# Kernel optimization log

Hardware: AMD Instinct MI355X
Metric: run time of the kernel (lower is better)

The kernel has to match this reference:

```python
import jax, jax.numpy as jnp
import numpy as np

B, S, H = 32, 4096, 16
QC, LORA, ROPE, NOPE, VH, DM = 1536, 512, 64, 128, 128, 2048
SCALE = 1.0 / np.sqrt(NOPE + ROPE)


def _rope(x, pos):
    # GPT-NeoX style rotary, dim=ROPE, base=10000. x: [B,H,ROPE] or [B,ROPE]
    half = ROPE // 2
    inv = 1.0 / (10000.0 ** (jnp.arange(half, dtype=jnp.float32) / half))
    f = pos.astype(jnp.float32)[:, None] * inv  # [B, half]
    cos, sin = jnp.cos(f), jnp.sin(f)
    if x.ndim == 3:
        cos, sin = cos[:, None, :], sin[:, None, :]
    x1, x2 = x[..., :half], x[..., half:]
    return jnp.concatenate([x1 * cos - x2 * sin, x2 * cos + x1 * sin], axis=-1)


def setup_inputs() -> dict:
    key = jax.random.key(0)
    ks = jax.random.split(key, 11)
    w = 0.02  # small init so logits are well-scaled
    return {
        "q_c": jax.random.normal(ks[0], (B, QC), jnp.float32),
        "k_c_normed": jax.random.normal(ks[1], (B, LORA), jnp.float32),
        "k_pe": jax.random.normal(ks[2], (B, ROPE), jnp.float32),
        "kv_c_cache": jax.random.normal(ks[3], (B, S, LORA), jnp.float32),
        "k_pe_cache": jax.random.normal(ks[4], (B, S, ROPE), jnp.float32),
        "W_UQ": jax.random.normal(ks[5], (QC, H, NOPE), jnp.float32) * w,
        "W_UK": jax.random.normal(ks[6], (LORA, H, NOPE), jnp.float32) * w,
        "W_QR": jax.random.normal(ks[7], (QC, H * ROPE), jnp.float32) * w,
        "W_UV": jax.random.normal(ks[8], (LORA, H, VH), jnp.float32) * w,
        "W_O": jax.random.normal(ks[9], (H * VH, DM), jnp.float32) * w,
        "input_positions": jnp.full((B,), S - 1, dtype=jnp.int32),
    }


def reference(q_c, k_c_normed, k_pe, kv_c_cache, k_pe_cache,
              W_UQ, W_UK, W_QR, W_UV, W_O, input_positions):
    pos = input_positions
    # matrix-absorbed q_nope: (q_c @ W_UQ) absorbed through W_UK -> latent space
    q_t = jnp.einsum('bd,dhn->bhn', q_c, W_UQ)            # [B,H,NOPE]
    q_nope = jnp.einsum('bhn,lhn->bhl', q_t, W_UK)        # [B,H,LORA]
    q_pe = _rope((q_c @ W_QR).reshape(B, H, ROPE), pos)   # [B,H,ROPE]
    k_pe_rot = _rope(k_pe, pos)                            # [B,ROPE]
    # write current latent token into cache (paged write flattened)
    b_idx = jnp.arange(B)
    kv_c = kv_c_cache.at[b_idx, pos].set(k_c_normed)       # [B,S,LORA]
    kp = k_pe_cache.at[b_idx, pos].set(k_pe_rot)           # [B,S,ROPE]
    # attention in latent space
    scores = (jnp.einsum('bhl,bsl->bhs', q_nope, kv_c)
              + jnp.einsum('bhr,bsr->bhs', q_pe, kp)) * SCALE
    attn = jax.nn.softmax(scores, axis=-1)                 # [B,H,S]
    o = jnp.einsum('bhs,bsl->bhl', attn, kv_c)             # [B,H,LORA]
    v = jnp.einsum('bhl,lhv->bhv', o, W_UV)                # [B,H,VH]
    out = v.reshape(B, H * VH) @ W_O                       # [B,DM]
    return out.reshape(B, 1, DM)
```

## Files before the change

### kernel.cpp

```cpp
#include <hip/hip_runtime.h>
#include <hip/hip_bf16.h>
#include <math.h>

#define B 32
#define S 4096
#define H 16
#define QC 1536
#define LORA 512
#define ROPE 64
#define NOPE 128
#define VH 128
#define DM 2048
#define NC 32
#define CHUNK (S / NC)
#define NKS 24
#define FLP 584

__device__ __constant__ float SCALE_C = 0.07216878364870323f;

typedef __attribute__((ext_vector_type(8))) short bf16x8;
typedef __attribute__((ext_vector_type(4))) float f32x4;

__device__ inline ushort f2b(float x) {
    union { float f; uint u; } v; v.f = x;
    return (ushort)((v.u + 0x7FFFu + ((v.u >> 16) & 1u)) >> 16);
}

__global__ __launch_bounds__(256) void k_proj_part(
    const float* __restrict__ q_c, const float* __restrict__ W_UQ,
    const float* __restrict__ W_QR, float* __restrict__ part) {
    const int ks = blockIdx.x, cs = blockIdx.y, t = threadIdx.x;
    const int k0 = ks * 64;
    __shared__ float qs[64][32];
    for (int i = t; i < 64 * 32; i += 256) {
        const int k = i >> 5, b2 = i & 31;
        qs[k][b2] = q_c[(size_t)b2 * QC + k0 + k];
    }
    __syncthreads();
    const int tc = t & 63, tb = t >> 6;
    const int col = cs * 256 + tc * 4;
    const float* W; int N, coll;
    if (cs < 8) { W = W_UQ; N = 2048; coll = col; }
    else        { W = W_QR; N = 1024; coll = col - 2048; }
    float4 acc[8];
#pragma unroll
    for (int i = 0; i < 8; i++) acc[i] = make_float4(0.f, 0.f, 0.f, 0.f);
#pragma unroll 4
    for (int k = 0; k < 64; ++k) {
        const float4 w4 = *(const float4*)(W + (size_t)(k0 + k) * N + coll);
        const float4 a1 = *(const float4*)&qs[k][tb * 8];
        const float4 a2 = *(const float4*)&qs[k][tb * 8 + 4];
        acc[0].x += a1.x * w4.x; acc[0].y += a1.x * w4.y; acc[0].z += a1.x * w4.z; acc[0].w += a1.x * w4.w;
        acc[1].x += a1.y * w4.x; acc[1].y += a1.y * w4.y; acc[1].z += a1.y * w4.z; acc[1].w += a1.y * w4.w;
        acc[2].x += a1.z * w4.x; acc[2].y += a1.z * w4.y; acc[2].z += a1.z * w4.z; acc[2].w += a1.z * w4.w;
        acc[3].x += a1.w * w4.x; acc[3].y += a1.w * w4.y; acc[3].z += a1.w * w4.z; acc[3].w += a1.w * w4.w;
        acc[4].x += a2.x * w4.x; acc[4].y += a2.x * w4.y; acc[4].z += a2.x * w4.z; acc[4].w += a2.x * w4.w;
        acc[5].x += a2.y * w4.x; acc[5].y += a2.y * w4.y; acc[5].z += a2.y * w4.z; acc[5].w += a2.y * w4.w;
        acc[6].x += a2.z * w4.x; acc[6].y += a2.z * w4.y; acc[6].z += a2.z * w4.z; acc[6].w += a2.z * w4.w;
        acc[7].x += a2.w * w4.x; acc[7].y += a2.w * w4.y; acc[7].z += a2.w * w4.z; acc[7].w += a2.w * w4.w;
    }
#pragma unroll
    for (int j = 0; j < 8; j++) {
        const int b2 = tb * 8 + j;
        *(float4*)(part + ((size_t)ks * 32 + b2) * 3072 + col) = acc[j];
    }
}

__global__ __launch_bounds__(256) void k_finalize(
    const float* __restrict__ part, const float* __restrict__ k_pe,
    const int* __restrict__ pos_arr, float* __restrict__ q_t,
    ushort* __restrict__ q_bf, float* __restrict__ kpe_rot) {
    const int blk = blockIdx.x, t = threadIdx.x;
    if (blk < 64) {
        const int idx = blk * 256 + t;
        const int b = idx >> 9, c4 = idx & 511;
        const int col = c4 * 4;
        float4 acc = make_float4(0.f, 0.f, 0.f, 0.f);
        for (int ks = 0; ks < NKS; ks++) {
            const float4 p = *(const float4*)(part + ((size_t)ks * 32 + b) * 3072 + col);
            acc.x += p.x; acc.y += p.y; acc.z += p.z; acc.w += p.w;
        }
        *(float4*)(q_t + (size_t)b * 2048 + col) = acc;
    } else if (blk < 80) {
        const int idx = (blk - 64) * 256 + t;
        const int b = idx >> 7, rest = idx & 127;
        const int h = rest >> 3, pr = rest & 7;
        const int col1 = 2048 + h * 64 + pr * 4;
        float x1[4] = {0.f, 0.f, 0.f, 0.f}, x2[4] = {0.f, 0.f, 0.f, 0.f};
        for (int ks = 0; ks < NKS; ks++) {
            const float* p = part + ((size_t)ks * 32 + b) * 3072;
            const float4 a = *(const float4*)(p + col1);
            const float4 c = *(const float4*)(p + col1 + 32);
            x1[0] += a.x; x1[1] += a.y; x1[2] += a.z; x1[3] += a.w;
            x2[0] += c.x; x2[1] += c.y; x2[2] += c.z; x2[3] += c.w;
        }
        const int pos = pos_arr[b];
        ushort* qb = q_bf + ((size_t)b * 16 + h) * 576 + 512 + pr * 4;
#pragma unroll
        for (int e = 0; e < 4; ++e) {
            const int j = pr * 4 + e;
            const double inv = pow(10000.0, -(double)j / 32.0);
            const double f = (double)pos * inv;
            const float cc = (float)cos(f), ss = (float)sin(f);
            qb[e] = f2b(x1[e] * cc - x2[e] * ss);
            qb[32 + e] = f2b(x2[e] * cc + x1[e] * ss);
        }
    } else {
        for (int i = t; i < 32 * 32; i += 256) {
            const int b = i >> 5, j = i & 31;
            const int pos = pos_arr[b];
            const double inv = pow(10000.0, -(double)j / 32.0);
            const double f = (double)pos * inv;
            const float cc = (float)cos(f), ss = (float)sin(f);
            const float x1 = k_pe[(size_t)b * 64 + j], x2 = k_pe[(size_t)b * 64 + j + 32];
            kpe_rot[(size_t)b * 64 + j] = x1 * cc - x2 * ss;
            kpe_rot[(size_t)b * 64 + j + 32] = x2 * cc + x1 * ss;
        }
    }
}

__global__ __launch_bounds__(256) void k_qnope(
    const float* __restrict__ q_t, const float* __restrict__ W_UK,
    ushort* __restrict__ q_bf) {
    const int l0 = blockIdx.x * 64, h = blockIdx.y;
    const int t = threadIdx.x;
    __shared__ float qs[32][NOPE];
    for (int i = t; i < 32 * NOPE; i += 256) {
        const int b2 = i >> 7, n = i & 127;
        qs[b2][n] = q_t[(size_t)b2 * 2048 + h * NOPE + n];
    }
    __syncthreads();
    const int wave = t >> 6, lane = t & 63;
    const int half = lane >> 5, nl = (lane & 31) * 4;
    for (int sw = 0; sw < 8; ++sw) {
        const int l = l0 + sw * 8 + wave * 2 + half;
        const float4 w4 = *(const float4*)(W_UK + ((size_t)l * H + h) * NOPE + nl);
        for (int b2 = 0; b2 < 32; ++b2) {
            const float4 a4 = *(const float4*)&qs[b2][nl];
            float d = a4.x * w4.x + a4.y * w4.y + a4.z * w4.z + a4.w * w4.w;
            d += __shfl_xor(d, 16);
            d += __shfl_xor(d, 8);
            d += __shfl_xor(d, 4);
            d += __shfl_xor(d, 2);
            d += __shfl_xor(d, 1);
            if ((lane & 31) == 0)
                q_bf[((size_t)b2 * 16 + h) * 576 + l] = f2b(d);
        }
    }
}

__global__ __launch_bounds__(256) void k_flash(
    const ushort* __restrict__ q_bf, const float* __restrict__ kv_cache,
    const float* __restrict__ kpe_cache, const float* __restrict__ k_c_normed,
    const float* __restrict__ kpe_rot, const int* __restrict__ pos_arr,
    float* __restrict__ part_o, float* __restrict__ part_ml) {
    __shared__ ushort k_lds[2][16][FLP];
    __shared__ uint p_lds[4][16][20];
    const int blk = blockIdx.x;
    const int b = blk / NC, c = blk % NC;
    const int t = threadIdx.x, lane = t & 63, wave = t >> 6;
    const int lg = lane >> 4, hd = lane & 15;
    const int pos = pos_arr[b];
    const int s0 = c * CHUNK;
    const int rel = pos - s0;
    const int pt = (rel >= 0 && rel < CHUNK) ? (rel >> 4) : -1;
    const int prow = rel & 15;

    const float* kv_b = kv_cache + (size_t)b * S * LORA;
    const float* kp_b = kpe_cache + (size_t)b * S * ROPE;
    const float* kc_b = k_c_normed + (size_t)b * LORA;
    const float* kr_b = kpe_rot + (size_t)b * ROPE;

    bf16x8 qf[18];
    {
        const ushort* qr = q_bf + ((size_t)b * 16 + hd) * 576 + lg * 8;
#pragma unroll
        for (int ks = 0; ks < 18; ++ks)
            qf[ks] = *(const bf16x8*)(qr + 32 * ks);
    }

    float4 ld[9];
    auto issue = [&](int tile) {
        const int r = t >> 4, f0 = t & 15;
        const int s = s0 + tile * 16 + r;
        const float* kvr = kv_b + (size_t)s * LORA;
        const float* per = kp_b + (size_t)s * ROPE;
#pragma unroll
        for (int k = 0; k < 8; ++k) ld[k] = *(const float4*)(kvr + 4 * (f0 + 16 * k));
        ld[8] = *(const float4*)(per + 4 * f0);
    };
    auto wtile = [&](int buf) {
        const int r = t >> 4, f0 = t & 15;
        ushort* dst = &k_lds[buf][r][0];
#pragma unroll
        for (int k = 0; k < 9; ++k) {
            const int f = f0 + 16 * k;
            ushort4 h4;
            h4.x = f2b(ld[k].x); h4.y = f2b(ld[k].y);
            h4.z = f2b(ld[k].z); h4.w = f2b(ld[k].w);
            *(ushort4*)(dst + 4 * f) = h4;
        }
    };
    auto patch = [&](int buf) {
        if (t < 144) {
            const float4 v = (t < 128) ? *(const float4*)(kc_b + 4 * t)
                                       : *(const float4*)(kr_b + 4 * (t - 128));
            ushort4 h4;
            h4.x = f2b(v.x); h4.y = f2b(v.y); h4.z = f2b(v.z); h4.w = f2b(v.w);
            *(ushort4*)(&k_lds[buf][prow][4 * t]) = h4;
        }
    };

    f32x4 acc[8];
#pragma unroll
    for (int i = 0; i < 8; ++i) acc[i] = (f32x4){0.f, 0.f, 0.f, 0.f};
    float m_run = -INFINITY, l_run = 0.f;

    issue(0);
    wtile(0);
    if (pt == 0) patch(0);
    __syncthreads();

    for (int tt = 0; tt < 8; ++tt) {
        if (tt < 7) issue(tt + 1);

        f32x4 S4 = (f32x4){0.f, 0.f, 0.f, 0.f};
        {
            const ushort* krow = &k_lds[tt & 1][hd][lg * 8];
#pragma unroll
            for (int ks = 0; ks < 18; ++ks) {
                const bf16x8 av = *(const bf16x8*)(krow + 32 * ks);
                S4 = __builtin_amdgcn_mfma_f32_16x16x32_bf16(av, qf[ks], S4, 0, 0, 0);
            }
        }
        const float sc0 = S4[0] * SCALE_C, sc1 = S4[1] * SCALE_C;
        const float sc2 = S4[2] * SCALE_C, sc3 = S4[3] * SCALE_C;

        float smax = fmaxf(fmaxf(sc0, sc1), fmaxf(sc2, sc3));
        smax = fmaxf(smax, __shfl_xor(smax, 16));
        smax = fmaxf(smax, __shfl_xor(smax, 32));
        const bool need = smax > m_run + 8.0f;
        if (__any(need)) {
            const float m_new = need ? smax : m_run;
            const float alpha = __expf(m_run - m_new);
            l_run *= alpha;
            m_run = m_new;
            const int hb = lg * 4;
            const float a0 = __shfl(alpha, hb + 0), a1 = __shfl(alpha, hb + 1);
            const float a2 = __shfl(alpha, hb + 2), a3 = __shfl(alpha, hb + 3);
#pragma unroll
            for (int d2 = 0; d2 < 8; ++d2) {
                acc[d2][0] *= a0; acc[d2][1] *= a1;
                acc[d2][2] *= a2; acc[d2][3] *= a3;
            }
        }
        const float p0 = __expf(sc0 - m_run), p1 = __expf(sc1 - m_run);
        const float p2 = __expf(sc2 - m_run), p3 = __expf(sc3 - m_run);
        float ps = p0 + p1 + p2 + p3;
        ps += __shfl_xor(ps, 16);
        ps += __shfl_xor(ps, 32);
        l_run += ps;
        const uint plo = (uint)f2b(p0) | ((uint)f2b(p1) << 16);
        const uint phi = (uint)f2b(p2) | ((uint)f2b(p3) << 16);
        *(uint2*)&p_lds[wave][hd][(tt & 1) * 8 + lg * 2] = make_uint2(plo, phi);

        if (tt & 1) {
            const bf16x8 ap = *(const bf16x8*)&p_lds[wave][hd][lg * 4];
            const int half = lane >> 5;
            const int rbase = (lg & 1) * 8;
#pragma unroll
            for (int dt = 0; dt < 8; ++dt) {
                const int dcol = wave * 128 + dt * 16 + hd;
                union { bf16x8 v; ushort u[8]; } bv;
#pragma unroll
                for (int i2 = 0; i2 < 8; ++i2)
                    bv.u[i2] = k_lds[half][rbase + i2][dcol];
                acc[dt] = __builtin_amdgcn_mfma_f32_16x16x32_bf16(ap, bv.v, acc[dt], 0, 0, 0);
            }
        }

        __syncthreads();
        if (tt < 7) {
            wtile((tt + 1) & 1);
            if (pt == tt + 1) patch((tt + 1) & 1);
        }
        __syncthreads();
    }

    float* po = part_o + ((size_t)(b * NC + c) * H) * LORA;
#pragma unroll
    for (int dt = 0; dt < 8; ++dt) {
        const int dim = wave * 128 + dt * 16 + hd;
        const int hb = lg * 4;
        po[(size_t)(hb + 0) * LORA + dim] = acc[dt][0];
        po[(size_t)(hb + 1) * LORA + dim] = acc[dt][1];
        po[(size_t)(hb + 2) * LORA + dim] = acc[dt][2];
        po[(size_t)(hb + 3) * LORA + dim] = acc[dt][3];
    }
    if (wave == 0 && lane < 16) {
        float* pml = part_ml + ((size_t)(b * NC + c) * H + lane) * 2;
        pml[0] = m_run;
        pml[1] = l_run;
    }
}

__global__ __launch_bounds__(256) void k_combine(
    const float* __restrict__ part_o, const float* __restrict__ part_ml,
    const float* __restrict__ W_UV, float* __restrict__ v) {
    const int b0 = blockIdx.x * 4, h = blockIdx.y, t = threadIdx.x;
    __shared__ float ml_s[4][NC][2];
    __shared__ float o_s[4][LORA];
    if (t < 256) {
        const int b2 = t >> 6, c = (t >> 1) & 31, w = t & 1;
        ml_s[b2][c][w] = part_ml[(((size_t)(b0 + b2) * NC + c) * H + h) * 2 + w];
    }
    __syncthreads();
    float m_b[4], inv_l[4];
#pragma unroll
    for (int b2 = 0; b2 < 4; ++b2) {
        float m = -INFINITY;
        for (int c = 0; c < NC; c++) m = fmaxf(m, ml_s[b2][c][0]);
        float l = 0.f;
        for (int c = 0; c < NC; c++) l += ml_s[b2][c][1] * __expf(ml_s[b2][c][0] - m);
        m_b[b2] = m;
        inv_l[b2] = 1.0f / l;
    }
    for (int i = t; i < 4 * LORA; i += 256) {
        const int b2 = i >> 9, li = i & 511;
        float acc = 0.f;
        for (int c = 0; c < NC; c++) {
            acc += part_o[(((size_t)(b0 + b2) * NC + c) * H + h) * LORA + li] *
                   __expf(ml_s[b2][c][0] - m_b[b2]);
        }
        o_s[b2][li] = acc * inv_l[b2];
    }
    __syncthreads();
    const int vi = t & 127, bp = t >> 7;
    float acc0 = 0.f, acc1 = 0.f;
    for (int l = 0; l < LORA; l += 4) {
        const float w0 = W_UV[(size_t)(l + 0) * (H * VH) + h * VH + vi];
        const float w1 = W_UV[(size_t)(l + 1) * (H * VH) + h * VH + vi];
        const float w2 = W_UV[(size_t)(l + 2) * (H * VH) + h * VH + vi];
        const float w3 = W_UV[(size_t)(l + 3) * (H * VH) + h * VH + vi];
        const float4 oa = *(const float4*)&o_s[bp * 2][l];
        const float4 ob = *(const float4*)&o_s[bp * 2 + 1][l];
        acc0 += oa.x * w0 + oa.y * w1 + oa.z * w2 + oa.w * w3;
        acc1 += ob.x * w0 + ob.y * w1 + ob.z * w2 + ob.w * w3;
    }
    v[(size_t)(b0 + bp * 2) * (H * VH) + h * VH + vi] = acc0;
    v[(size_t)(b0 + bp * 2 + 1) * (H * VH) + h * VH + vi] = acc1;
}

__global__ void k_out(const float* __restrict__ v, const float* __restrict__ W_O,
                      float* __restrict__ out_part) {
    const int dsl = blockIdx.x, ksl = blockIdx.y, t = threadIdx.x;
    const int d0 = dsl * 128, k0 = ksl * 128;
    __shared__ float vs[32][128];
    for (int i = t; i < 32 * 128; i += 256) {
        const int bi = i >> 7, kk = i & 127;
        vs[bi][kk] = v[(size_t)bi * DM + k0 + kk];
    }
    __syncthreads();
    const int dl = t & 127, bh = t >> 7;
    float acc[16];
#pragma unroll
    for (int i = 0; i < 16; i++) acc[i] = 0.f;
    for (int kk = 0; kk < 128; kk += 4) {
        const float w0 = W_O[(size_t)(k0 + kk + 0) * DM + d0 + dl];
        const float w1 = W_O[(size_t)(k0 + kk + 1) * DM + d0 + dl];
        const float w2 = W_O[(size_t)(k0 + kk + 2) * DM + d0 + dl];
        const float w3 = W_O[(size_t)(k0 + kk + 3) * DM + d0 + dl];
#pragma unroll
        for (int i = 0; i < 16; i++) {
            const float4 vv = *(const float4*)&vs[bh * 16 + i][kk];
            acc[i] += vv.x * w0 + vv.y * w1 + vv.z * w2 + vv.w * w3;
        }
    }
    float* op = out_part + (size_t)ksl * 32 * DM;
#pragma unroll
    for (int i = 0; i < 16; i++) op[(size_t)(bh * 16 + i) * DM + d0 + dl] = acc[i];
}

__global__ void k_out_reduce(const float* __restrict__ out_part, float* __restrict__ out) {
    const int idx = blockIdx.x * 256 + threadIdx.x;
    float4 acc = make_float4(0.f, 0.f, 0.f, 0.f);
    for (int ks = 0; ks < 16; ks++) {
        float4 p = *(const float4*)(out_part + (size_t)ks * (32 * DM) + (size_t)idx * 4);
        acc.x += p.x; acc.y += p.y; acc.z += p.z; acc.w += p.w;
    }
    *(float4*)(out + (size_t)idx * 4) = acc;
}

extern "C" void kernel_launch(void* const* d_in, const int* in_sizes, int n_in,
                              void* d_out, int out_size, void* d_ws, size_t ws_size,
                              hipStream_t stream) {
    const float* q_c        = (const float*)d_in[0];
    const float* k_c_normed = (const float*)d_in[1];
    const float* k_pe       = (const float*)d_in[2];
    const float* kv_c_cache = (const float*)d_in[3];
    const float* k_pe_cache = (const float*)d_in[4];
    const float* W_UQ       = (const float*)d_in[5];
    const float* W_UK       = (const float*)d_in[6];
    const float* W_QR       = (const float*)d_in[7];
    const float* W_UV       = (const float*)d_in[8];
    const float* W_O        = (const float*)d_in[9];
    const int*   pos        = (const int*)d_in[10];

    float* ws = (float*)d_ws;
    float* q_t       = ws;
    float* qbf_f     = q_t + 65536;
    ushort* q_bf     = (ushort*)qbf_f;
    float* kpe_rot   = qbf_f + 147456;
    float* part_o    = kpe_rot + 2048;
    float* part_ml   = part_o + (size_t)B * NC * H * LORA;
    float* v         = part_ml + (size_t)B * NC * H * 2;
    float* out_part  = v + 65536;
    float* proj_part = out_part + (size_t)16 * 32 * DM;

    k_proj_part<<<dim3(NKS, 12), 256, 0, stream>>>(q_c, W_UQ, W_QR, proj_part);
    k_finalize<<<81, 256, 0, stream>>>(proj_part, k_pe, pos, q_t, q_bf, kpe_rot);
    k_qnope<<<dim3(8, 16), 256, 0, stream>>>(q_t, W_UK, q_bf);
    k_flash<<<B * NC, 256, 0, stream>>>(q_bf, kv_c_cache, k_pe_cache,
                                        k_c_normed, kpe_rot, pos, part_o, part_ml);
    k_combine<<<dim3(8, 16), 256, 0, stream>>>(part_o, part_ml, W_UV, v);
    k_out<<<dim3(16, 16), 256, 0, stream>>>(v, W_O, out_part);
    k_out_reduce<<<64, 256, 0, stream>>>(out_part, (float*)d_out);
}
```

Before: 226.4 us.

## Triple-buffer LDS tiles with two register prefetch sets in flash kernel

The flash-decode chunk loop now uses three LDS buffers and two register staging arrays, so the next tile is written to LDS right after the current tile's compute without an extra barrier. This removes one __syncthreads per tile and keeps global loads two tiles ahead. In exchange it uses more LDS and doubles the prefetch registers, which may lower occupancy.

```diff
diff --git a/kernel.cpp b/kernel.cpp
--- a/kernel.cpp
+++ b/kernel.cpp
@@ -154,7 +154,7 @@
     const float* __restrict__ kpe_cache, const float* __restrict__ k_c_normed,
     const float* __restrict__ kpe_rot, const int* __restrict__ pos_arr,
     float* __restrict__ part_o, float* __restrict__ part_ml) {
-    __shared__ ushort k_lds[2][16][FLP];
+    __shared__ ushort k_lds[3][16][FLP];
     __shared__ uint p_lds[4][16][20];
     const int blk = blockIdx.x;
     const int b = blk / NC, c = blk % NC;
@@ -179,8 +179,8 @@
             qf[ks] = *(const bf16x8*)(qr + 32 * ks);
     }
 
-    float4 ld[9];
-    auto issue = [&](int tile) {
+    float4 ldA[9], ldB[9];
+    auto issue = [&](int tile, float4 (&ld)[9]) {
         const int r = t >> 4, f0 = t & 15;
         const int s = s0 + tile * 16 + r;
         const float* kvr = kv_b + (size_t)s * LORA;
@@ -189,7 +189,7 @@
         for (int k = 0; k < 8; ++k) ld[k] = *(const float4*)(kvr + 4 * (f0 + 16 * k));
         ld[8] = *(const float4*)(per + 4 * f0);
     };
-    auto wtile = [&](int buf) {
+    auto wtile = [&](float4 (&ld)[9], int buf) {
         const int r = t >> 4, f0 = t & 15;
         ushort* dst = &k_lds[buf][r][0];
 #pragma unroll
@@ -216,17 +216,10 @@
     for (int i = 0; i < 8; ++i) acc[i] = (f32x4){0.f, 0.f, 0.f, 0.f};
     float m_run = -INFINITY, l_run = 0.f;
 
-    issue(0);
-    wtile(0);
-    if (pt == 0) patch(0);
-    __syncthreads();
-
-    for (int tt = 0; tt < 8; ++tt) {
-        if (tt < 7) issue(tt + 1);
-
+    auto compute = [&](int tt) {
         f32x4 S4 = (f32x4){0.f, 0.f, 0.f, 0.f};
         {
-            const ushort* krow = &k_lds[tt & 1][hd][lg * 8];
+            const ushort* krow = &k_lds[tt % 3][hd][lg * 8];
 #pragma unroll
             for (int ks = 0; ks < 18; ++ks) {
                 const bf16x8 av = *(const bf16x8*)(krow + 32 * ks);
@@ -267,6 +260,7 @@
         if (tt & 1) {
             const bf16x8 ap = *(const bf16x8*)&p_lds[wave][hd][lg * 4];
             const int half = lane >> 5;
+            const int bsel = (tt - 1 + half) % 3;
             const int rbase = (lg & 1) * 8;
 #pragma unroll
             for (int dt = 0; dt < 8; ++dt) {
@@ -274,15 +268,29 @@
                 union { bf16x8 v; ushort u[8]; } bv;
 #pragma unroll
                 for (int i2 = 0; i2 < 8; ++i2)
-                    bv.u[i2] = k_lds[half][rbase + i2][dcol];
+                    bv.u[i2] = k_lds[bsel][rbase + i2][dcol];
                 acc[dt] = __builtin_amdgcn_mfma_f32_16x16x32_bf16(ap, bv.v, acc[dt], 0, 0, 0);
             }
         }
-
+    };
+
+    issue(0, ldB);
+    wtile(ldB, 0);
+    if (pt == 0) patch(0);
+    issue(1, ldA);
+    __syncthreads();
+
+    for (int tb = 0; tb < 8; tb += 2) {
+        if (tb + 2 < 8) issue(tb + 2, ldB);
+        compute(tb);
+        wtile(ldA, (tb + 1) % 3);
+        if (pt == tb + 1) patch((tb + 1) % 3);
         __syncthreads();
-        if (tt < 7) {
-            wtile((tt + 1) & 1);
-            if (pt == tt + 1) patch((tt + 1) & 1);
+        if (tb + 3 < 8) issue(tb + 3, ldA);
+        compute(tb + 1);
+        if (tb + 2 < 8) {
+            wtile(ldB, (tb + 2) % 3);
+            if (pt == tb + 2) patch((tb + 2) % 3);
         }
         __syncthreads();
     }
```

Result: faster. 217.0 us (-4.2%).
